# Performance work log

Hardware: AMD Instinct MI355X
Metric: run time of the kernel (lower is better)

## Reference

```python
import jax, jax.numpy as jnp
import numpy as np

S, D_IN, D = 4, 1024, 256   # n_scales, input dim, d_per_scale (d_model=1024)
B, T = 4, 4096
R_MIN, R_MAX, TH_MIN, TH_MAX = 0.9, 0.999, 0.01, 1.0


def setup_inputs() -> dict:
    key = jax.random.key(0)
    ks = jax.random.split(key, 6)
    s_in = 1.0 / np.sqrt(D_IN)
    s_h = 1.0 / np.sqrt(D)
    return {
        'x':   jax.random.normal(ks[0], (B, T, D_IN), jnp.float32),
        'Wg1': jax.random.normal(ks[1], (S, D_IN, D), jnp.float32) * s_in,
        'bg1': jnp.zeros((S, D), jnp.float32),
        'Wg2': jax.random.normal(ks[2], (S, D, D), jnp.float32) * s_h,
        'bg2': jnp.full((S, D), -4.0, jnp.float32),  # bias_init=constant(-4.0)
        'Wdr': jax.random.normal(ks[3], (S, D_IN, D), jnp.float32) * s_in,
        'bdr': jnp.zeros((S, D), jnp.float32),
        'Wdi': jax.random.normal(ks[4], (S, D_IN, D), jnp.float32) * s_in,
        'bdi': jnp.zeros((S, D), jnp.float32),
    }


def _scale_consts():
    r = np.concatenate([[1.0], np.linspace(R_MAX, R_MIN, S - 1)])
    theta = np.concatenate([[0.0], np.linspace(TH_MIN, TH_MAX, S - 1)])
    a_base = (r * np.exp(1j * theta)).astype(np.complex64)        # (S,)
    bscale = np.where(r >= 1.0, 1.0 / np.sqrt(D), 1.0 - r).astype(np.float32)  # (S,)
    return jnp.asarray(a_base), jnp.asarray(bscale)


def reference(x, Wg1, bg1, Wg2, bg2, Wdr, bdr, Wdi, bdi):
    a_base, bscale = _scale_consts()
    # gate MLP (conditioning = x): (B,S,T,D)
    g1 = jax.nn.relu(jnp.einsum('bti,sid->bstd', x, Wg1) + bg1[None, :, None, :])
    gate = jax.nn.sigmoid(jnp.einsum('bstd,sde->bste', g1, Wg2) + bg2[None, :, None, :])
    # complex drive
    dre = jnp.einsum('bti,sid->bstd', x, Wdr) + bdr[None, :, None, :]
    dim = jnp.einsum('bti,sid->bstd', x, Wdi) + bdi[None, :, None, :]
    omg = (1.0 - gate).astype(jnp.complex64)                       # (B,S,T,D)
    a = omg * a_base[None, :, None, None]
    b = omg * ((dre + 1j * dim).astype(jnp.complex64) * bscale[None, :, None, None])
    # linear recurrence h_t = a_t*h_{t-1} + b_t via associative scan along time
    def binop(left, right):
        al, bl = left
        ar, br = right
        return (al * ar, ar * bl + br)
    _, h = jax.lax.associative_scan(binop, (a, b), axis=2)         # (B,S,T,D)
    h = jnp.moveaxis(h, 1, 2)                                      # (B,T,S,D)
    out = jnp.stack([h.real, h.imag], axis=3)                      # (B,T,S,2,D) -> re/im per scale
    return out.reshape(B, T, S * 2 * D)
```

## Files before the change

kernel.cpp:

```cpp
#include <hip/hip_runtime.h>
#include <cmath>

#define S_   4
#define DIN  1024
#define D_   256
#define B_   4
#define T_   4096
#define BT_  (B_*T_)
#define GN   (S_*3*D_)
#define CHUNKS 128
#define CL   (T_/CHUNKS)

typedef short bf16x8 __attribute__((ext_vector_type(8)));
typedef float f32x4  __attribute__((ext_vector_type(4)));

struct SC { float are[S_]; float aim[S_]; float bsc[S_]; };

__device__ inline unsigned short f2bf(float f) {
    unsigned int u = __builtin_bit_cast(unsigned int, f);
    unsigned int r = (u + 0x7FFFu + ((u >> 16) & 1u)) >> 16;
    return (unsigned short)r;
}
__device__ inline float bf2f_lo(unsigned int u) {
    return __builtin_bit_cast(float, u << 16);
}
__device__ inline float bf2f_hi(unsigned int u) {
    return __builtin_bit_cast(float, u & 0xFFFF0000u);
}
__device__ inline float u16om(unsigned int u) {
    return ((float)u + 0.5f) * (1.f/65536.f);
}

#define GLD_LDS(gp, lp) \
    __builtin_amdgcn_global_load_lds( \
        (const __attribute__((address_space(1))) void*)(gp), \
        (__attribute__((address_space(3))) void*)(lp), 16, 0, 0)

__global__ __launch_bounds__(256) void kconv_x(
    const float* __restrict__ x, unsigned short* __restrict__ xb)
{
    const size_t i = ((size_t)blockIdx.x*256 + threadIdx.x)*4;
    const float4 v = *(const float4*)(x + i);
    ushort4 o;
    o.x = f2bf(v.x); o.y = f2bf(v.y); o.z = f2bf(v.z); o.w = f2bf(v.w);
    *(ushort4*)(xb + i) = o;
}

__global__ __launch_bounds__(256) void kconv_w(
    const float* __restrict__ src, unsigned short* __restrict__ dst,
    int K, int N, size_t dst_s_stride)
{
    __shared__ float t[32][33];
    const int k0 = blockIdx.x*32, n0 = blockIdx.y*32, s = blockIdx.z;
    const float* sp = src + (size_t)s*K*N;
    unsigned short* dp = dst + (size_t)s*dst_s_stride;
    const int c = threadIdx.x & 31, r0 = threadIdx.x >> 5;
    #pragma unroll
    for (int p = 0; p < 4; ++p)
        t[r0 + p*8][c] = sp[(size_t)(k0 + r0 + p*8)*N + n0 + c];
    __syncthreads();
    #pragma unroll
    for (int p = 0; p < 4; ++p)
        dp[(size_t)(n0 + r0 + p*8)*K + k0 + c] = f2bf(t[c][r0 + p*8]);
}

template<bool DRVB>
__global__ __launch_bounds__(256) void k1_mfma(
    const unsigned short* __restrict__ xb,
    const unsigned short* __restrict__ Bct,
    const float* __restrict__ bg1, const float* __restrict__ bdr,
    const float* __restrict__ bdi,
    unsigned short* __restrict__ g1b,
    unsigned short* __restrict__ drvb, float* __restrict__ drvf)
{
    __shared__ unsigned short As[128*64];
    __shared__ unsigned short Bs[128*64];

    const int tid = threadIdx.x;
    const int wave = tid >> 6, lane = tid & 63;
    const int wm = (wave >> 1) * 64, wn = (wave & 1) * 64;
    const int row0 = blockIdx.x * 128, col0 = blockIdx.y * 128;

    const f32x4 z = {0.f, 0.f, 0.f, 0.f};
    f32x4 acc[4][4];
    #pragma unroll
    for (int i = 0; i < 4; ++i)
        #pragma unroll
        for (int j = 0; j < 4; ++j) acc[i][j] = z;

    const unsigned short* Ag = xb  + (size_t)row0*DIN;
    const unsigned short* Bg = Bct + (size_t)col0*DIN;
    const int lrow = lane >> 3;
    const int lksw = ((lane & 7) ^ lrow) * 8;
    const int cn   = lane & 15, quad = lane >> 4;
    const int e    = cn & 7;

    for (int k0 = 0; k0 < DIN; k0 += 64) {
        #pragma unroll
        for (int t = 0; t < 4; ++t) {
            const int m0 = wave*32 + t*8;
            GLD_LDS(Ag + (size_t)(m0 + lrow)*DIN + k0 + lksw, As + m0*64);
            GLD_LDS(Bg + (size_t)(m0 + lrow)*DIN + k0 + lksw, Bs + m0*64);
        }
        __syncthreads();
        #pragma unroll
        for (int ks = 0; ks < 2; ++ks) {
            const int offs = (((ks*4 + quad) ^ e)) * 8;
            bf16x8 af[4], bfv[4];
            #pragma unroll
            for (int i = 0; i < 4; ++i)
                af[i] = *(const bf16x8*)(As + (wm + i*16 + cn)*64 + offs);
            #pragma unroll
            for (int j = 0; j < 4; ++j)
                bfv[j] = *(const bf16x8*)(Bs + (wn + j*16 + cn)*64 + offs);
            #pragma unroll
            for (int i = 0; i < 4; ++i)
                #pragma unroll
                for (int j = 0; j < 4; ++j)
                    acc[i][j] = __builtin_amdgcn_mfma_f32_16x16x32_bf16(
                        af[i], bfv[j], acc[i][j], 0, 0, 0);
        }
        __syncthreads();
    }

    const int s    = col0 / 768;
    const int rem  = col0 - s*768;
    const int mat  = rem >> 8;
    const int dbase = (rem & 255) + wn + cn;
    const float* bias = (mat == 0) ? bg1 : ((mat == 1) ? bdr : bdi);
    float bv[4];
    #pragma unroll
    for (int j = 0; j < 4; ++j) bv[j] = bias[s*D_ + dbase + j*16];

    const int qr = quad * 4;
    #pragma unroll
    for (int i = 0; i < 4; ++i) {
        const int m = row0 + wm + i*16 + qr;
        #pragma unroll
        for (int j = 0; j < 4; ++j) {
            const int d = dbase + j*16;
            const f32x4 v = acc[i][j];
            if (mat == 0) {
                unsigned short* gp = g1b + ((size_t)s*BT_ + m)*D_ + d;
                #pragma unroll
                for (int r = 0; r < 4; ++r)
                    gp[(size_t)r*D_] = f2bf(fmaxf(v[r] + bv[j], 0.f));
            } else {
                const size_t base = (size_t)m*(S_*2*D_) + s*2*D_
                                  + (mat == 2 ? D_ : 0) + d;
                if (DRVB) {
                    #pragma unroll
                    for (int r = 0; r < 4; ++r)
                        drvb[base + (size_t)r*(S_*2*D_)] = f2bf(v[r] + bv[j]);
                } else {
                    #pragma unroll
                    for (int r = 0; r < 4; ++r)
                        drvf[base + (size_t)r*(S_*2*D_)] = v[r] + bv[j];
                }
            }
        }
    }
}

__global__ __launch_bounds__(256) void k2_mfma(
    const unsigned short* __restrict__ g1b,
    const unsigned short* __restrict__ B2t,
    const float* __restrict__ bg2, unsigned short* __restrict__ omgu)
{
    __shared__ unsigned short As[128*64];
    __shared__ unsigned short Bs[128*64];

    const int tid = threadIdx.x;
    const int wave = tid >> 6, lane = tid & 63;
    const int wm = (wave >> 1) * 64, wn = (wave & 1) * 64;
    const int row0 = blockIdx.x * 128, col0 = blockIdx.y * 128;
    const int s = blockIdx.z;

    const f32x4 z = {0.f, 0.f, 0.f, 0.f};
    f32x4 acc[4][4];
    #pragma unroll
    for (int i = 0; i < 4; ++i)
        #pragma unroll
        for (int j = 0; j < 4; ++j) acc[i][j] = z;

    const unsigned short* Ag = g1b + ((size_t)s*BT_ + row0)*D_;
    const unsigned short* Bg = B2t + (size_t)s*D_*D_ + (size_t)col0*D_;
    const int lrow = lane >> 3;
    const int lksw = ((lane & 7) ^ lrow) * 8;
    const int cn   = lane & 15, quad = lane >> 4;
    const int e    = cn & 7;

    for (int k0 = 0; k0 < D_; k0 += 64) {
        #pragma unroll
        for (int t = 0; t < 4; ++t) {
            const int m0 = wave*32 + t*8;
            GLD_LDS(Ag + (size_t)(m0 + lrow)*D_ + k0 + lksw, As + m0*64);
            GLD_LDS(Bg + (size_t)(m0 + lrow)*D_ + k0 + lksw, Bs + m0*64);
        }
        __syncthreads();
        #pragma unroll
        for (int ks = 0; ks < 2; ++ks) {
            const int offs = (((ks*4 + quad) ^ e)) * 8;
            bf16x8 af[4], bfv[4];
            #pragma unroll
            for (int i = 0; i < 4; ++i)
                af[i] = *(const bf16x8*)(As + (wm + i*16 + cn)*64 + offs);
            #pragma unroll
            for (int j = 0; j < 4; ++j)
                bfv[j] = *(const bf16x8*)(Bs + (wn + j*16 + cn)*64 + offs);
            #pragma unroll
            for (int i = 0; i < 4; ++i)
                #pragma unroll
                for (int j = 0; j < 4; ++j)
                    acc[i][j] = __builtin_amdgcn_mfma_f32_16x16x32_bf16(
                        af[i], bfv[j], acc[i][j], 0, 0, 0);
        }
        __syncthreads();
    }

    const int qr = quad * 4;
    float bv[4];
    #pragma unroll
    for (int j = 0; j < 4; ++j) bv[j] = bg2[s*D_ + col0 + wn + j*16 + cn];

    #pragma unroll
    for (int i = 0; i < 4; ++i) {
        const int m = row0 + wm + i*16 + qr;
        #pragma unroll
        for (int j = 0; j < 4; ++j) {
            const int d = col0 + wn + j*16 + cn;
            const f32x4 v = acc[i][j];
            unsigned short* op = omgu + ((size_t)s*BT_ + m)*D_ + d;
            #pragma unroll
            for (int r = 0; r < 4; ++r) {
                const float om = 1.f / (1.f + __expf(v[r] + bv[j]));
                op[(size_t)r*D_] =
                    (unsigned short)fminf(om * 65536.f, 65535.f);
            }
        }
    }
}

template<bool DRVB>
__global__ __launch_bounds__(128) void k3a_chunk(
    const unsigned short* __restrict__ omgu,
    const unsigned short* __restrict__ drvb, const float* __restrict__ drvf,
    float4* __restrict__ summ, SC sc)
{
    const int blk = blockIdx.x;
    const int c = blk & (CHUNKS-1);
    const int s = (blk >> 7) & (S_-1);
    const int b = blk >> 9;
    const int d2 = threadIdx.x;

    const float are = sc.are[s], aim = sc.aim[s], bs = sc.bsc[s];
    float Ar[2] = {1.f,1.f}, Ai[2] = {0,0}, Hr[2] = {0,0}, Hi[2] = {0,0};
    const int t0 = c * CL;

    #pragma unroll 4
    for (int t = 0; t < CL; ++t) {
        const int bt = b*T_ + t0 + t;
        const unsigned int ov =
            *(const unsigned int*)(omgu + ((size_t)s*BT_ + bt)*D_ + 2*d2);
        const float om[2] = { u16om(ov & 0xFFFFu), u16om(ov >> 16) };
        const size_t base = (size_t)bt*(S_*2*D_) + s*2*D_ + 2*d2;
        float dre[2], dim[2];
        if (DRVB) {
            const unsigned int ur = *(const unsigned int*)(drvb + base);
            const unsigned int ui = *(const unsigned int*)(drvb + base + D_);
            dre[0] = bf2f_lo(ur); dre[1] = bf2f_hi(ur);
            dim[0] = bf2f_lo(ui); dim[1] = bf2f_hi(ui);
        } else {
            const float2 fr = *(const float2*)(drvf + base);
            const float2 fi = *(const float2*)(drvf + base + D_);
            dre[0] = fr.x; dre[1] = fr.y; dim[0] = fi.x; dim[1] = fi.y;
        }
        #pragma unroll
        for (int u = 0; u < 2; ++u) {
            const float ar = om[u]*are, ai = om[u]*aim, ob = om[u]*bs;
            const float br = ob*dre[u], bi = ob*dim[u];
            const float nHr = ar*Hr[u] - ai*Hi[u] + br;
            const float nHi = ar*Hi[u] + ai*Hr[u] + bi;
            const float nAr = ar*Ar[u] - ai*Ai[u];
            const float nAi = ar*Ai[u] + ai*Ar[u];
            Hr[u]=nHr; Hi[u]=nHi; Ar[u]=nAr; Ai[u]=nAi;
        }
    }
    const size_t so = ((size_t)(b*S_ + s)*CHUNKS + c)*D_ + 2*d2;
    summ[so]     = make_float4(Ar[0], Ai[0], Hr[0], Hi[0]);
    summ[so + 1] = make_float4(Ar[1], Ai[1], Hr[1], Hi[1]);
}

__global__ __launch_bounds__(256) void k3b_scan(float4* __restrict__ summ)
{
    const int idx = blockIdx.x*256 + threadIdx.x;
    const int d = idx & (D_-1);
    const int s = (idx >> 8) & (S_-1);
    const int b = idx >> 10;

    float cr = 0.f, ci = 0.f;
    for (int c = 0; c < CHUNKS; ++c) {
        const size_t off = ((size_t)(b*S_ + s)*CHUNKS + c)*D_ + d;
        const float4 v = summ[off];
        const float ncr = v.x*cr - v.y*ci + v.z;
        const float nci = v.x*ci + v.y*cr + v.w;
        *(float2*)&summ[off] = make_float2(cr, ci);
        cr = ncr; ci = nci;
    }
}

template<bool DRVB>
__global__ __launch_bounds__(128) void k3c_final(
    const unsigned short* __restrict__ omgu,
    const unsigned short* __restrict__ drvb, const float* __restrict__ drvf,
    float* __restrict__ out, const float4* __restrict__ summ, SC sc)
{
    const int blk = blockIdx.x;
    const int c = blk & (CHUNKS-1);
    const int s = (blk >> 7) & (S_-1);
    const int b = blk >> 9;
    const int d2 = threadIdx.x;

    const float are = sc.are[s], aim = sc.aim[s], bs = sc.bsc[s];
    const size_t so = ((size_t)(b*S_ + s)*CHUNKS + c)*D_ + 2*d2;
    const float4 v0 = summ[so];
    const float4 v1 = summ[so + 1];
    float Hr[2] = {v0.x, v1.x}, Hi[2] = {v0.y, v1.y};
    const int t0 = c * CL;

    #pragma unroll 4
    for (int t = 0; t < CL; ++t) {
        const int bt = b*T_ + t0 + t;
        const unsigned int ov =
            *(const unsigned int*)(omgu + ((size_t)s*BT_ + bt)*D_ + 2*d2);
        const float om[2] = { u16om(ov & 0xFFFFu), u16om(ov >> 16) };
        const size_t base = (size_t)bt*(S_*2*D_) + s*2*D_ + 2*d2;
        float dre[2], dim[2];
        if (DRVB) {
            const unsigned int ur = *(const unsigned int*)(drvb + base);
            const unsigned int ui = *(const unsigned int*)(drvb + base + D_);
            dre[0] = bf2f_lo(ur); dre[1] = bf2f_hi(ur);
            dim[0] = bf2f_lo(ui); dim[1] = bf2f_hi(ui);
        } else {
            const float2 fr = *(const float2*)(drvf + base);
            const float2 fi = *(const float2*)(drvf + base + D_);
            dre[0] = fr.x; dre[1] = fr.y; dim[0] = fi.x; dim[1] = fi.y;
        }
        #pragma unroll
        for (int u = 0; u < 2; ++u) {
            const float ar = om[u]*are, ai = om[u]*aim, ob = om[u]*bs;
            const float br = ob*dre[u], bi = ob*dim[u];
            const float nHr = ar*Hr[u] - ai*Hi[u] + br;
            const float nHi = ar*Hi[u] + ai*Hr[u] + bi;
            Hr[u]=nHr; Hi[u]=nHi;
        }
        *(float2*)(out + base)      = make_float2(Hr[0], Hr[1]);
        *(float2*)(out + base + D_) = make_float2(Hi[0], Hi[1]);
    }
}

extern "C" void kernel_launch(void* const* d_in, const int* in_sizes, int n_in,
                              void* d_out, int out_size, void* d_ws, size_t ws_size,
                              hipStream_t stream)
{
    const float* x   = (const float*)d_in[0];
    const float* Wg1 = (const float*)d_in[1];
    const float* bg1 = (const float*)d_in[2];
    const float* Wg2 = (const float*)d_in[3];
    const float* bg2 = (const float*)d_in[4];
    const float* Wdr = (const float*)d_in[5];
    const float* bdr = (const float*)d_in[6];
    const float* Wdi = (const float*)d_in[7];
    const float* bdi = (const float*)d_in[8];
    float* out = (float*)d_out;

    char* ws = (char*)d_ws;
    unsigned short* g1b  = (unsigned short*)(ws + 0);
    float4*         summ = (float4*)(ws + 0);
    unsigned short* B2t  = (unsigned short*)(ws + 33554432);
    unsigned short* xb   = (unsigned short*)(ws + 34078720);
    unsigned short* omgu = (unsigned short*)(ws + 34078720);
    unsigned short* Bct  = (unsigned short*)(ws + 67633152);
    unsigned short* drvb = (unsigned short*)(ws + 73924608);
    const bool drv_bf16 = ws_size >= (size_t)73924608 + 67108864;

    SC sc;
    {
        const double r[S_]  = {1.0, 0.999, 0.9495, 0.9};
        const double th[S_] = {0.0, 0.01, 0.505, 1.0};
        for (int s = 0; s < S_; ++s) {
            sc.are[s] = (float)(r[s] * cos(th[s]));
            sc.aim[s] = (float)(r[s] * sin(th[s]));
            sc.bsc[s] = (r[s] >= 1.0) ? (float)(1.0/16.0) : (float)(1.0 - r[s]);
        }
    }

    kconv_x<<<(BT_*DIN)/1024, 256, 0, stream>>>(x, xb);
    kconv_w<<<dim3(32,8,S_), 256, 0, stream>>>(Wg1, Bct + 0*D_*DIN, DIN, D_, (size_t)768*DIN);
    kconv_w<<<dim3(32,8,S_), 256, 0, stream>>>(Wdr, Bct + 1*D_*DIN, DIN, D_, (size_t)768*DIN);
    kconv_w<<<dim3(32,8,S_), 256, 0, stream>>>(Wdi, Bct + 2*D_*DIN, DIN, D_, (size_t)768*DIN);
    kconv_w<<<dim3(8,8,S_),  256, 0, stream>>>(Wg2, B2t, D_, D_, (size_t)D_*D_);

    if (drv_bf16)
        k1_mfma<true><<<dim3(BT_/128, GN/128), 256, 0, stream>>>(
            xb, Bct, bg1, bdr, bdi, g1b, drvb, out);
    else
        k1_mfma<false><<<dim3(BT_/128, GN/128), 256, 0, stream>>>(
            xb, Bct, bg1, bdr, bdi, g1b, drvb, out);
    k2_mfma<<<dim3(BT_/128, D_/128, S_), 256, 0, stream>>>(g1b, B2t, bg2, omgu);

    if (drv_bf16) {
        k3a_chunk<true><<<B_*S_*CHUNKS, 128, 0, stream>>>(omgu, drvb, out, summ, sc);
        k3b_scan       <<<(B_*S_*D_)/256, 256, 0, stream>>>(summ);
        k3c_final<true><<<B_*S_*CHUNKS, 128, 0, stream>>>(omgu, drvb, out, out, summ, sc);
    } else {
        k3a_chunk<false><<<B_*S_*CHUNKS, 128, 0, stream>>>(omgu, drvb, out, summ, sc);
        k3b_scan        <<<(B_*S_*D_)/256, 256, 0, stream>>>(summ);
        k3c_final<false><<<B_*S_*CHUNKS, 128, 0, stream>>>(omgu, drvb, out, out, summ, sc);
    }
}
```

Measured before the change: 429.4 us.

## Pipeline main GEMM with 256x256 tiles, parallelize chunk scan, fuse weight conversions

The first projection GEMM moves to 512-thread blocks with 256x256 output tiles and an 8-phase double-buffered LDS pipeline. Global-to-LDS prefetch is interleaved with MFMA work, using explicit waitcnt, barriers and setprio. The cross-chunk carry scan changes from one serial loop per channel into a parallel Hillis-Steele scan in shared memory, with 128 threads per channel. Three weight-conversion launches become one kernel. The larger tile uses 128KB of LDS and many accumulator registers, and the scan does more total work, so occupancy and register pressure may suffer.

After: 406.6 us. 5.3% less time.

```diff
diff --git a/kernel.cpp b/kernel.cpp
--- a/kernel.cpp
+++ b/kernel.cpp
@@ -64,8 +64,29 @@
         dp[(size_t)(n0 + r0 + p*8)*K + k0 + c] = f2bf(t[c][r0 + p*8]);
 }
 
+__global__ __launch_bounds__(256) void kconv_w3(
+    const float* __restrict__ Wg1, const float* __restrict__ Wdr,
+    const float* __restrict__ Wdi, unsigned short* __restrict__ dst)
+{
+    __shared__ float t[32][33];
+    const int z = blockIdx.z;
+    const int widx = z >> 2, s = z & 3;
+    const float* src = (widx == 0) ? Wg1 : ((widx == 1) ? Wdr : Wdi);
+    const float* sp = src + (size_t)s*DIN*D_;
+    unsigned short* dp = dst + (size_t)s*768*DIN + (size_t)widx*D_*DIN;
+    const int k0 = blockIdx.x*32, n0 = blockIdx.y*32;
+    const int c = threadIdx.x & 31, r0 = threadIdx.x >> 5;
+    #pragma unroll
+    for (int p = 0; p < 4; ++p)
+        t[r0 + p*8][c] = sp[(size_t)(k0 + r0 + p*8)*D_ + n0 + c];
+    __syncthreads();
+    #pragma unroll
+    for (int p = 0; p < 4; ++p)
+        dp[(size_t)(n0 + r0 + p*8)*DIN + k0 + c] = f2bf(t[c][r0 + p*8]);
+}
+
 template<bool DRVB>
-__global__ __launch_bounds__(256) void k1_mfma(
+__global__ __launch_bounds__(512, 2) void k1_8p(
     const unsigned short* __restrict__ xb,
     const unsigned short* __restrict__ Bct,
     const float* __restrict__ bg1, const float* __restrict__ bdr,
@@ -73,72 +94,117 @@
     unsigned short* __restrict__ g1b,
     unsigned short* __restrict__ drvb, float* __restrict__ drvf)
 {
-    __shared__ unsigned short As[128*64];
-    __shared__ unsigned short Bs[128*64];
-
-    const int tid = threadIdx.x;
+    __shared__ unsigned short L[8*8192];
+
+    const int tid  = threadIdx.x;
     const int wave = tid >> 6, lane = tid & 63;
-    const int wm = (wave >> 1) * 64, wn = (wave & 1) * 64;
-    const int row0 = blockIdx.x * 128, col0 = blockIdx.y * 128;
-
+    const int wmr  = wave >> 2;
+    const int wnr  = wave & 3;
+    const int row0 = blockIdx.x * 256, col0 = blockIdx.y * 256;
+    const int cn = lane & 15, quad = lane >> 4;
+    const int e8 = cn & 7;
+    const int srow = lane >> 3;
+    const int lksw = ((lane & 7) ^ srow) * 8;
+
+    const unsigned short* Ag = xb  + (size_t)row0 * DIN;
+    const unsigned short* Bg = Bct + (size_t)col0 * DIN;
+
+    f32x4 acc[8][4];
     const f32x4 z = {0.f, 0.f, 0.f, 0.f};
-    f32x4 acc[4][4];
-    #pragma unroll
-    for (int i = 0; i < 4; ++i)
+    #pragma unroll
+    for (int i = 0; i < 8; ++i)
         #pragma unroll
         for (int j = 0; j < 4; ++j) acc[i][j] = z;
 
-    const unsigned short* Ag = xb  + (size_t)row0*DIN;
-    const unsigned short* Bg = Bct + (size_t)col0*DIN;
-    const int lrow = lane >> 3;
-    const int lksw = ((lane & 7) ^ lrow) * 8;
-    const int cn   = lane & 15, quad = lane >> 4;
-    const int e    = cn & 7;
-
-    for (int k0 = 0; k0 < DIN; k0 += 64) {
-        #pragma unroll
-        for (int t = 0; t < 4; ++t) {
-            const int m0 = wave*32 + t*8;
-            GLD_LDS(Ag + (size_t)(m0 + lrow)*DIN + k0 + lksw, As + m0*64);
-            GLD_LDS(Bg + (size_t)(m0 + lrow)*DIN + k0 + lksw, Bs + m0*64);
-        }
-        __syncthreads();
-        #pragma unroll
-        for (int ks = 0; ks < 2; ++ks) {
-            const int offs = (((ks*4 + quad) ^ e)) * 8;
-            bf16x8 af[4], bfv[4];
-            #pragma unroll
-            for (int i = 0; i < 4; ++i)
-                af[i] = *(const bf16x8*)(As + (wm + i*16 + cn)*64 + offs);
-            #pragma unroll
-            for (int j = 0; j < 4; ++j)
-                bfv[j] = *(const bf16x8*)(Bs + (wn + j*16 + cn)*64 + offs);
-            #pragma unroll
-            for (int i = 0; i < 4; ++i)
-                #pragma unroll
-                for (int j = 0; j < 4; ++j)
-                    acc[i][j] = __builtin_amdgcn_mfma_f32_16x16x32_bf16(
-                        af[i], bfv[j], acc[i][j], 0, 0, 0);
-        }
-        __syncthreads();
-    }
+#define SLOT(b,o,h) (L + (((b)*4 + (o)*2 + (h)) * 8192))
+#define STAGE(b,o,h,kt,Gp) do { \
+    const unsigned short* _g = (Gp) + (size_t)((h)*128 + wave*8 + srow)*DIN \
+                             + (size_t)(kt)*64 + lksw; \
+    unsigned short* _l = SLOT(b,o,h) + wave*512; \
+    GLD_LDS(_g, _l); \
+    GLD_LDS(_g + (size_t)64*DIN, _l + 4096); \
+} while(0)
+
+#define PHASE(b, ih, jh, STG, WT) do { \
+    bf16x8 af[4][2], bfv[2][2]; \
+    _Pragma("unroll") \
+    for (int ii = 0; ii < 4; ++ii) { \
+        const unsigned short* ap = SLOT(b,0,ih) + (size_t)(wmr*64 + ii*16 + cn)*64; \
+        _Pragma("unroll") \
+        for (int kk = 0; kk < 2; ++kk) \
+            af[ii][kk] = *(const bf16x8*)(ap + ((kk*4 + quad) ^ e8)*8); \
+    } \
+    _Pragma("unroll") \
+    for (int jj = 0; jj < 2; ++jj) { \
+        const unsigned short* bp = SLOT(b,1,jh) + (size_t)(wnr*32 + jj*16 + cn)*64; \
+        _Pragma("unroll") \
+        for (int kk = 0; kk < 2; ++kk) \
+            bfv[jj][kk] = *(const bf16x8*)(bp + ((kk*4 + quad) ^ e8)*8); \
+    } \
+    STG; \
+    WT; \
+    __builtin_amdgcn_s_barrier(); \
+    asm volatile("s_waitcnt lgkmcnt(0)" ::: "memory"); \
+    __builtin_amdgcn_s_setprio(1); \
+    _Pragma("unroll") \
+    for (int ii = 0; ii < 4; ++ii) \
+        _Pragma("unroll") \
+        for (int jj = 0; jj < 2; ++jj) \
+            _Pragma("unroll") \
+            for (int kk = 0; kk < 2; ++kk) \
+                acc[(ih)*4 + ii][(jh)*2 + jj] = \
+                    __builtin_amdgcn_mfma_f32_16x16x32_bf16( \
+                        af[ii][kk], bfv[jj][kk], \
+                        acc[(ih)*4 + ii][(jh)*2 + jj], 0, 0, 0); \
+    __builtin_amdgcn_s_setprio(0); \
+    __builtin_amdgcn_s_barrier(); \
+} while(0)
+
+    STAGE(0,0,0, 0, Ag); STAGE(0,1,0, 0, Bg);
+    STAGE(0,0,1, 0, Ag); STAGE(0,1,1, 0, Bg);
+    STAGE(1,0,0, 1, Ag); STAGE(1,1,1, 1, Bg);
+    asm volatile("s_waitcnt vmcnt(4)" ::: "memory");
+    __builtin_amdgcn_s_barrier();
+
+    #pragma unroll 1
+    for (int it = 0; it < 8; ++it) {
+        const int t1 = 2*it + 1, t2 = 2*it + 2, t3 = 2*it + 3;
+        const bool pf = (it < 7);
+        PHASE(0, 0, 0, { STAGE(1,0,1, t1, Ag); }, {});
+        PHASE(0, 0, 1, { STAGE(1,1,0, t1, Bg); }, {});
+        PHASE(0, 1, 1, { if (pf) STAGE(0,0,0, t2, Ag); }, {});
+        PHASE(0, 1, 0, { if (pf) STAGE(0,1,1, t2, Bg); },
+              { if (pf) asm volatile("s_waitcnt vmcnt(4)" ::: "memory");
+                else    asm volatile("s_waitcnt vmcnt(0)" ::: "memory"); });
+        PHASE(1, 0, 0, { if (pf) STAGE(0,0,1, t2, Ag); }, {});
+        PHASE(1, 0, 1, { if (pf) STAGE(0,1,0, t2, Bg); }, {});
+        PHASE(1, 1, 1, { if (pf) STAGE(1,0,0, t3, Ag); }, {});
+        PHASE(1, 1, 0, { if (pf) STAGE(1,1,1, t3, Bg); },
+              { if (pf) asm volatile("s_waitcnt vmcnt(4)" ::: "memory");
+                else    asm volatile("s_waitcnt vmcnt(0)" ::: "memory"); });
+    }
+#undef PHASE
+#undef STAGE
+#undef SLOT
 
     const int s    = col0 / 768;
     const int rem  = col0 - s*768;
     const int mat  = rem >> 8;
-    const int dbase = (rem & 255) + wn + cn;
     const float* bias = (mat == 0) ? bg1 : ((mat == 1) ? bdr : bdi);
-    float bv[4];
-    #pragma unroll
-    for (int j = 0; j < 4; ++j) bv[j] = bias[s*D_ + dbase + j*16];
-
-    const int qr = quad * 4;
-    #pragma unroll
-    for (int i = 0; i < 4; ++i) {
-        const int m = row0 + wm + i*16 + qr;
+
+    int dloc[4]; float bv[4];
+    #pragma unroll
+    for (int j = 0; j < 4; ++j) {
+        dloc[j] = (j >> 1)*128 + wnr*32 + (j & 1)*16 + cn;
+        bv[j] = bias[s*D_ + dloc[j]];
+    }
+
+    #pragma unroll
+    for (int i = 0; i < 8; ++i) {
+        const int m = row0 + (i >> 2)*128 + wmr*64 + (i & 3)*16 + quad*4;
         #pragma unroll
         for (int j = 0; j < 4; ++j) {
-            const int d = dbase + j*16;
+            const int d = dloc[j];
             const f32x4 v = acc[i][j];
             if (mat == 0) {
                 unsigned short* gp = g1b + ((size_t)s*BT_ + m)*D_ + d;
@@ -293,20 +359,37 @@
 
 __global__ __launch_bounds__(256) void k3b_scan(float4* __restrict__ summ)
 {
-    const int idx = blockIdx.x*256 + threadIdx.x;
-    const int d = idx & (D_-1);
-    const int s = (idx >> 8) & (S_-1);
-    const int b = idx >> 10;
-
-    float cr = 0.f, ci = 0.f;
-    for (int c = 0; c < CHUNKS; ++c) {
-        const size_t off = ((size_t)(b*S_ + s)*CHUNKS + c)*D_ + d;
-        const float4 v = summ[off];
-        const float ncr = v.x*cr - v.y*ci + v.z;
-        const float nci = v.x*ci + v.y*cr + v.w;
-        *(float2*)&summ[off] = make_float2(cr, ci);
-        cr = ncr; ci = nci;
-    }
+    __shared__ float4 sb[2][CHUNKS];
+    const int ch = threadIdx.x >> 7;
+    const int c  = threadIdx.x & (CHUNKS-1);
+    const int channel = blockIdx.x*2 + ch;
+    const int d = channel & (D_-1);
+    const int s = (channel >> 8) & (S_-1);
+    const int b = channel >> 10;
+    const size_t off = ((size_t)(b*S_ + s)*CHUNKS + c)*D_ + d;
+
+    float4 v = summ[off];
+    sb[ch][c] = v;
+    __syncthreads();
+    #pragma unroll
+    for (int st = 1; st < CHUNKS; st <<= 1) {
+        float4 l;
+        if (c >= st) l = sb[ch][c - st];
+        __syncthreads();
+        if (c >= st) {
+            float4 nv;
+            nv.x = l.x*v.x - l.y*v.y;
+            nv.y = l.x*v.y + l.y*v.x;
+            nv.z = v.x*l.z - v.y*l.w + v.z;
+            nv.w = v.x*l.w + v.y*l.z + v.w;
+            v = nv;
+            sb[ch][c] = v;
+        }
+        __syncthreads();
+    }
+    float2 carry = make_float2(0.f, 0.f);
+    if (c > 0) { const float4 p = sb[ch][c-1]; carry = make_float2(p.z, p.w); }
+    *(float2*)&summ[off] = carry;
 }
 
 template<bool DRVB>
@@ -396,26 +479,24 @@
     }
 
     kconv_x<<<(BT_*DIN)/1024, 256, 0, stream>>>(x, xb);
-    kconv_w<<<dim3(32,8,S_), 256, 0, stream>>>(Wg1, Bct + 0*D_*DIN, DIN, D_, (size_t)768*DIN);
-    kconv_w<<<dim3(32,8,S_), 256, 0, stream>>>(Wdr, Bct + 1*D_*DIN, DIN, D_, (size_t)768*DIN);
-    kconv_w<<<dim3(32,8,S_), 256, 0, stream>>>(Wdi, Bct + 2*D_*DIN, DIN, D_, (size_t)768*DIN);
+    kconv_w3<<<dim3(32,8,12), 256, 0, stream>>>(Wg1, Wdr, Wdi, Bct);
     kconv_w<<<dim3(8,8,S_),  256, 0, stream>>>(Wg2, B2t, D_, D_, (size_t)D_*D_);
 
     if (drv_bf16)
-        k1_mfma<true><<<dim3(BT_/128, GN/128), 256, 0, stream>>>(
+        k1_8p<true><<<dim3(BT_/256, GN/256), 512, 0, stream>>>(
             xb, Bct, bg1, bdr, bdi, g1b, drvb, out);
     else
-        k1_mfma<false><<<dim3(BT_/128, GN/128), 256, 0, stream>>>(
+        k1_8p<false><<<dim3(BT_/256, GN/256), 512, 0, stream>>>(
             xb, Bct, bg1, bdr, bdi, g1b, drvb, out);
     k2_mfma<<<dim3(BT_/128, D_/128, S_), 256, 0, stream>>>(g1b, B2t, bg2, omgu);
 
     if (drv_bf16) {
         k3a_chunk<true><<<B_*S_*CHUNKS, 128, 0, stream>>>(omgu, drvb, out, summ, sc);
-        k3b_scan       <<<(B_*S_*D_)/256, 256, 0, stream>>>(summ);
+        k3b_scan       <<<(B_*S_*D_)/2, 256, 0, stream>>>(summ);
         k3c_final<true><<<B_*S_*CHUNKS, 128, 0, stream>>>(omgu, drvb, out, out, summ, sc);
     } else {
         k3a_chunk<false><<<B_*S_*CHUNKS, 128, 0, stream>>>(omgu, drvb, out, summ, sc);
-        k3b_scan        <<<(B_*S_*D_)/256, 256, 0, stream>>>(summ);
+        k3b_scan        <<<(B_*S_*D_)/2, 256, 0, stream>>>(summ);
         k3c_final<false><<<B_*S_*CHUNKS, 128, 0, stream>>>(omgu, drvb, out, out, summ, sc);
     }
 }
```
